# Kernel optimization log

Measured on AMD Instinct MI355X. Metric: run time of the kernel, lower is better.

The kernel has to match this reference:

```python
import jax, jax.numpy as jnp
import numpy as np

KH = KW = 3
PAD = 1

def _patches(x):
    # x: [B, C, H, W] -> periodic pad then 3x3 patches [B, C, KH, KW, H, W]
    B, C, H, W = x.shape
    xp = jnp.pad(x, ((0, 0), (0, 0), (PAD, PAD), (PAD, PAD)), mode='wrap')
    rows = []
    for i in range(KH):
        cols = [xp[:, :, i:i + H, j:j + W] for j in range(KW)]
        rows.append(jnp.stack(cols, axis=2))  # [B, C, KW, H, W]
    return jnp.stack(rows, axis=2)  # [B, C, KH, KW, H, W]

def setup_inputs() -> dict:
    key = jax.random.key(0)
    k1, k2, k3 = jax.random.split(key, 3)
    B, C, O, H, W = 16, 64, 64, 128, 128
    input = jax.random.normal(k1, (B, C, H, W), dtype=jnp.float32)
    weight = jax.random.normal(k2, (B, C * KH * KW, O), dtype=jnp.float32) * 0.05
    bias = jax.random.normal(k3, (B, O), dtype=jnp.float32) * 0.05
    return {"input": input, "weight": weight, "bias": bias}

def reference(input, weight, bias):
    B, C, H, W = input.shape
    O = weight.shape[-1]
    p = _patches(input)  # [B, C, KH, KW, H, W]
    w = weight.reshape(B, C, KH, KW, O)
    # per-sample dynamic conv: contract over (C, KH, KW)
    y = jnp.einsum('bcijhw,bcijo->bohw', p, w)
    return y + bias[:, :, None, None]
```

## Files before the change

kernel.cpp:

```cpp
#include <hip/hip_runtime.h>
#include <stdint.h>

#define B_N 16
#define C_N 64
#define O_N 64
#define H_N 128
#define W_N 128

typedef short bf16x8 __attribute__((ext_vector_type(8)));
typedef float f32x4 __attribute__((ext_vector_type(4)));
typedef unsigned short u16;
typedef u16 u16x4 __attribute__((ext_vector_type(4)));
typedef u16 u16x8 __attribute__((ext_vector_type(8)));

__device__ __forceinline__ u16 f2bf(float f) {
    uint32_t u = __float_as_uint(f);
    u += 0x7FFFu + ((u >> 16) & 1u);
    return (u16)(u >> 16);
}

__device__ __forceinline__ int swz(int w) { return (w & 7) << 4; }

__global__ __launch_bounds__(512, 2) void conv_main(const float* __restrict__ x,
                                                    const float* __restrict__ wt,
                                                    const float* __restrict__ bias,
                                                    float* __restrict__ y) {
    __shared__ u16 xl[6 * 128 * 64];

    const int lid = (blockIdx.x & 7) * 32 + (blockIdx.x >> 3);
    const int b   = lid >> 4;
    const int h0  = (lid & 15) * 8;
    const int tid = threadIdx.x;
    const int wid = tid >> 6;
    const int l   = tid & 63;
    const int wave_m = wid >> 1;
    const int wave_n = wid & 1;
    const int m0 = wave_m * 32;
    const int o0 = wave_n * 32;
    const int lr = l & 15;
    const int lg = l >> 4;

    const int w4 = tid & 31;
    const int cq = tid >> 5;
    const float* xb  = x  + (size_t)b * (64 * 128 * 128);
    const float* wtb = wt + (size_t)b * (576 * 64);

    auto ldrow = [&](int s, f32x4* d) {
        int hr = (h0 + s + 127) & 127;
        const float* src = xb + ((size_t)cq * 4 * 128 + hr) * 128 + w4 * 4;
        d[0] = *reinterpret_cast<const f32x4*>(src);
        d[1] = *reinterpret_cast<const f32x4*>(src + 16384);
        d[2] = *reinterpret_cast<const f32x4*>(src + 32768);
        d[3] = *reinterpret_cast<const f32x4*>(src + 49152);
    };
    auto wrrow = [&](int slot, const f32x4* d) {
#pragma unroll
        for (int j = 0; j < 4; ++j) {
            int w = w4 * 4 + j;
            u16x4 pk;
            pk.x = f2bf(d[0][j]); pk.y = f2bf(d[1][j]);
            pk.z = f2bf(d[2][j]); pk.w = f2bf(d[3][j]);
            int byte = slot * 16384 + w * 128 + ((cq * 8) ^ swz(w));
            *reinterpret_cast<u16x4*>(reinterpret_cast<char*>(xl) + byte) = pk;
        }
    };

    f32x4 s0[4], s1[4], s2[4], st[4];
    ldrow(0, s0); ldrow(1, s1); ldrow(2, s2);

    u16* wl = xl;
#pragma unroll
    for (int it = 0; it < 9; ++it) {
        int task = it * 512 + tid;
        int tl = task & 63;
        int of = (task >> 6) & 3;
        int cs = (task >> 8) & 1;
        int ij = task >> 9;
        const int o = of * 16 + (tl & 15);
        const int cbase = cs * 32 + (tl >> 4) * 8;
        u16x8 pk;
#pragma unroll
        for (int j8 = 0; j8 < 8; ++j8) {
            float v = wtb[(size_t)(cbase + j8) * 9 * 64 + (size_t)ij * 64 + o];
            pk[j8] = f2bf(v);
        }
        *reinterpret_cast<u16x8*>(wl + (size_t)task * 8) = pk;
    }
    __syncthreads();

    bf16x8 wreg[9][2][2];
#pragma unroll
    for (int ij = 0; ij < 9; ++ij)
#pragma unroll
        for (int cs = 0; cs < 2; ++cs)
#pragma unroll
            for (int nf = 0; nf < 2; ++nf)
                wreg[ij][cs][nf] = *reinterpret_cast<const bf16x8*>(
                    wl + (size_t)(((ij * 2 + cs) * 4 + wave_n * 2 + nf) * 64 + l) * 8);

    const float bv0 = bias[b * 64 + o0 + lr];
    const float bv1 = bias[b * 64 + o0 + 16 + lr];
    __syncthreads();

    wrrow(0, s0); wrrow(1, s1); wrrow(2, s2);
    ldrow(3, s0); ldrow(4, st);
    wrrow(3, s0);
    __syncthreads();

    int slA = 0;
#pragma unroll 1
    for (int r = 0; r < 8; ++r) {
        const int slB = (slA + 1 == 6) ? 0 : slA + 1;
        const int slC = (slB + 1 == 6) ? 0 : slB + 1;
        const int slW = (slC + 2 >= 6) ? slC + 2 - 6 : slC + 2;
        const int base0 = slA * 16384, base1 = slB * 16384, base2 = slC * 16384;

        f32x4 acc[2][2];
#pragma unroll
        for (int mf = 0; mf < 2; ++mf)
#pragma unroll
            for (int nf = 0; nf < 2; ++nf)
                acc[mf][nf] = (f32x4){0.f, 0.f, 0.f, 0.f};

#pragma unroll
        for (int ij = 0; ij < 9; ++ij) {
            if (ij == 0 && r < 6) wrrow(slW, st);
            if (ij == 3 && r < 5) ldrow(r + 5, st);

            const int i = ij / 3;
            const int jsh = ij % 3 - 1;
            const int rbase = (i == 0) ? base0 : (i == 1) ? base1 : base2;
#pragma unroll
            for (int cs = 0; cs < 2; ++cs) {
                const int cb = cs * 64 + lg * 16;
                bf16x8 afr[2];
#pragma unroll
                for (int mf = 0; mf < 2; ++mf) {
                    int w = (m0 + mf * 16 + lr + jsh + 128) & 127;
                    int byte = rbase + w * 128 + (cb ^ swz(w));
                    afr[mf] = *reinterpret_cast<const bf16x8*>(
                        reinterpret_cast<const char*>(xl) + byte);
                }
#pragma unroll
                for (int mf = 0; mf < 2; ++mf) {
                    acc[mf][0] = __builtin_amdgcn_mfma_f32_16x16x32_bf16(afr[mf], wreg[ij][cs][0], acc[mf][0], 0, 0, 0);
                    acc[mf][1] = __builtin_amdgcn_mfma_f32_16x16x32_bf16(afr[mf], wreg[ij][cs][1], acc[mf][1], 0, 0, 0);
                }
            }
        }

        const int h = h0 + r;
#pragma unroll
        for (int nf = 0; nf < 2; ++nf) {
            int o = o0 + nf * 16 + lr;
            float bv = nf ? bv1 : bv0;
#pragma unroll
            for (int mf = 0; mf < 2; ++mf) {
                int w0 = m0 + mf * 16 + lg * 4;
                float* dst = y + (((size_t)b * 64 + o) * 128 + h) * 128 + w0;
                f32x4 out;
                out[0] = acc[mf][nf][0] + bv;
                out[1] = acc[mf][nf][1] + bv;
                out[2] = acc[mf][nf][2] + bv;
                out[3] = acc[mf][nf][3] + bv;
                *reinterpret_cast<f32x4*>(dst) = out;
            }
        }

        if ((r & 1) && r < 7) __syncthreads();
        slA = slB;
    }
}

extern "C" void kernel_launch(void* const* d_in, const int* in_sizes, int n_in,
                              void* d_out, int out_size, void* d_ws, size_t ws_size,
                              hipStream_t stream) {
    const float* x    = (const float*)d_in[0];
    const float* wt   = (const float*)d_in[1];
    const float* bias = (const float*)d_in[2];
    float* y = (float*)d_out;
    (void)d_ws; (void)ws_size;

    hipLaunchKernelGGL(conv_main, dim3(B_N * H_N / 8), dim3(512), 0, stream,
                       x, wt, bias, y);
}
```

Before: 32.58 us.

## Reuse each staged input row across three output rows with rotating accumulators

Restructures the main loop to iterate over input rows instead of output rows. Each LDS-loaded A fragment feeds the MFMAs of up to three output rows, held in three rotating accumulator sets. This cuts LDS reads per output roughly threefold. It also fully unrolls the schedule and relaxes launch bounds to one block per SM, which raises register pressure and lowers occupancy.

```diff
diff --git a/kernel.cpp b/kernel.cpp
--- a/kernel.cpp
+++ b/kernel.cpp
@@ -21,7 +21,7 @@
 
 __device__ __forceinline__ int swz(int w) { return (w & 7) << 4; }
 
-__global__ __launch_bounds__(512, 2) void conv_main(const float* __restrict__ x,
+__global__ __launch_bounds__(512, 1) void conv_main(const float* __restrict__ x,
                                                     const float* __restrict__ wt,
                                                     const float* __restrict__ bias,
                                                     float* __restrict__ y) {
@@ -107,29 +107,25 @@
     wrrow(3, s0);
     __syncthreads();
 
-    int slA = 0;
-#pragma unroll 1
-    for (int r = 0; r < 8; ++r) {
-        const int slB = (slA + 1 == 6) ? 0 : slA + 1;
-        const int slC = (slB + 1 == 6) ? 0 : slB + 1;
-        const int slW = (slC + 2 >= 6) ? slC + 2 - 6 : slC + 2;
-        const int base0 = slA * 16384, base1 = slB * 16384, base2 = slC * 16384;
-
-        f32x4 acc[2][2];
+    f32x4 acc[3][2][2];
+#pragma unroll
+    for (int a = 0; a < 3; ++a)
 #pragma unroll
         for (int mf = 0; mf < 2; ++mf)
 #pragma unroll
             for (int nf = 0; nf < 2; ++nf)
-                acc[mf][nf] = (f32x4){0.f, 0.f, 0.f, 0.f};
-
-#pragma unroll
-        for (int ij = 0; ij < 9; ++ij) {
-            if (ij == 0 && r < 6) wrrow(slW, st);
-            if (ij == 3 && r < 5) ldrow(r + 5, st);
-
-            const int i = ij / 3;
-            const int jsh = ij % 3 - 1;
-            const int rbase = (i == 0) ? base0 : (i == 1) ? base1 : base2;
+                acc[a][mf][nf] = (f32x4){0.f, 0.f, 0.f, 0.f};
+
+#pragma unroll
+    for (int s = 0; s < 10; ++s) {
+        if (s <= 5) wrrow((s + 4) % 6, st);
+
+        const int rbase = (s % 6) * 16384;
+#pragma unroll
+        for (int jp = 0; jp < 3; ++jp) {
+            if (jp == 1 && s <= 4) ldrow(s + 5, st);
+
+            const int jsh = jp - 1;
 #pragma unroll
             for (int cs = 0; cs < 2; ++cs) {
                 const int cb = cs * 64 + lg * 16;
@@ -142,33 +138,53 @@
                         reinterpret_cast<const char*>(xl) + byte);
                 }
 #pragma unroll
-                for (int mf = 0; mf < 2; ++mf) {
-                    acc[mf][0] = __builtin_amdgcn_mfma_f32_16x16x32_bf16(afr[mf], wreg[ij][cs][0], acc[mf][0], 0, 0, 0);
-                    acc[mf][1] = __builtin_amdgcn_mfma_f32_16x16x32_bf16(afr[mf], wreg[ij][cs][1], acc[mf][1], 0, 0, 0);
+                for (int i = 0; i < 3; ++i) {
+                    const int r = s - i;
+                    if (r >= 0 && r <= 7) {
+                        const int a = r % 3;
+                        const int ij = i * 3 + jp;
+#pragma unroll
+                        for (int mf = 0; mf < 2; ++mf) {
+                            acc[a][mf][0] = __builtin_amdgcn_mfma_f32_16x16x32_bf16(
+                                afr[mf], wreg[ij][cs][0], acc[a][mf][0], 0, 0, 0);
+                            acc[a][mf][1] = __builtin_amdgcn_mfma_f32_16x16x32_bf16(
+                                afr[mf], wreg[ij][cs][1], acc[a][mf][1], 0, 0, 0);
+                        }
+                    }
                 }
             }
         }
 
-        const int h = h0 + r;
-#pragma unroll
-        for (int nf = 0; nf < 2; ++nf) {
-            int o = o0 + nf * 16 + lr;
-            float bv = nf ? bv1 : bv0;
-#pragma unroll
-            for (int mf = 0; mf < 2; ++mf) {
-                int w0 = m0 + mf * 16 + lg * 4;
-                float* dst = y + (((size_t)b * 64 + o) * 128 + h) * 128 + w0;
-                f32x4 out;
-                out[0] = acc[mf][nf][0] + bv;
-                out[1] = acc[mf][nf][1] + bv;
-                out[2] = acc[mf][nf][2] + bv;
-                out[3] = acc[mf][nf][3] + bv;
-                *reinterpret_cast<f32x4*>(dst) = out;
+        if (s >= 2) {
+            const int r = s - 2;
+            const int a = r % 3;
+            const int h = h0 + r;
+#pragma unroll
+            for (int nf = 0; nf < 2; ++nf) {
+                int o = o0 + nf * 16 + lr;
+                float bv = nf ? bv1 : bv0;
+#pragma unroll
+                for (int mf = 0; mf < 2; ++mf) {
+                    int w0 = m0 + mf * 16 + lg * 4;
+                    float* dst = y + (((size_t)b * 64 + o) * 128 + h) * 128 + w0;
+                    f32x4 out;
+                    out[0] = acc[a][mf][nf][0] + bv;
+                    out[1] = acc[a][mf][nf][1] + bv;
+                    out[2] = acc[a][mf][nf][2] + bv;
+                    out[3] = acc[a][mf][nf][3] + bv;
+                    *reinterpret_cast<f32x4*>(dst) = out;
+                }
             }
-        }
-
-        if ((r & 1) && r < 7) __syncthreads();
-        slA = slB;
+            if (r + 3 <= 7) {
+#pragma unroll
+                for (int mf = 0; mf < 2; ++mf)
+#pragma unroll
+                    for (int nf = 0; nf < 2; ++nf)
+                        acc[a][mf][nf] = (f32x4){0.f, 0.f, 0.f, 0.f};
+            }
+        }
+
+        if ((s & 1) && s < 9) __syncthreads();
     }
 }
 
```

Measured after the change: 55.82 us. 71.3% more time.

## Halve block to 4 waves, each computing all 64 output channels

Applied to the files above, without the earlier changes.

Block size drops from 512 to 256 threads. Each wave now covers 32 pixels by all 64 output channels instead of 32 by 32, which doubles weight registers and accumulators per wave. The row loads and stores are split into two halves per thread, and the weight staging loop runs 18 iterations. This raises per-thread register pressure (wreg grows to 72 bf16x8 vectors). Fewer waves are available to hide memory latency, in exchange for reusing each A fragment across more MFMAs.

```diff
diff --git a/kernel.cpp b/kernel.cpp
--- a/kernel.cpp
+++ b/kernel.cpp
@@ -21,7 +21,7 @@
 
 __device__ __forceinline__ int swz(int w) { return (w & 7) << 4; }
 
-__global__ __launch_bounds__(512, 2) void conv_main(const float* __restrict__ x,
+__global__ __launch_bounds__(256, 1) void conv_main(const float* __restrict__ x,
                                                     const float* __restrict__ wt,
                                                     const float* __restrict__ bias,
                                                     float* __restrict__ y) {
@@ -33,45 +33,49 @@
     const int tid = threadIdx.x;
     const int wid = tid >> 6;
     const int l   = tid & 63;
-    const int wave_m = wid >> 1;
-    const int wave_n = wid & 1;
-    const int m0 = wave_m * 32;
-    const int o0 = wave_n * 32;
-    const int lr = l & 15;
-    const int lg = l >> 4;
+    const int m0  = wid * 32;
+    const int lr  = l & 15;
+    const int lg  = l >> 4;
 
-    const int w4 = tid & 31;
-    const int cq = tid >> 5;
+    const int w4  = tid & 31;
+    const int cq2 = tid >> 5;
     const float* xb  = x  + (size_t)b * (64 * 128 * 128);
     const float* wtb = wt + (size_t)b * (576 * 64);
 
     auto ldrow = [&](int s, f32x4* d) {
         int hr = (h0 + s + 127) & 127;
-        const float* src = xb + ((size_t)cq * 4 * 128 + hr) * 128 + w4 * 4;
-        d[0] = *reinterpret_cast<const f32x4*>(src);
-        d[1] = *reinterpret_cast<const f32x4*>(src + 16384);
-        d[2] = *reinterpret_cast<const f32x4*>(src + 32768);
-        d[3] = *reinterpret_cast<const f32x4*>(src + 49152);
+#pragma unroll
+        for (int half = 0; half < 2; ++half) {
+            const float* src = xb + ((size_t)(cq2 * 2 + half) * 4 * 128 + hr) * 128 + w4 * 4;
+            d[half * 4 + 0] = *reinterpret_cast<const f32x4*>(src);
+            d[half * 4 + 1] = *reinterpret_cast<const f32x4*>(src + 16384);
+            d[half * 4 + 2] = *reinterpret_cast<const f32x4*>(src + 32768);
+            d[half * 4 + 3] = *reinterpret_cast<const f32x4*>(src + 49152);
+        }
     };
     auto wrrow = [&](int slot, const f32x4* d) {
 #pragma unroll
-        for (int j = 0; j < 4; ++j) {
-            int w = w4 * 4 + j;
-            u16x4 pk;
-            pk.x = f2bf(d[0][j]); pk.y = f2bf(d[1][j]);
-            pk.z = f2bf(d[2][j]); pk.w = f2bf(d[3][j]);
-            int byte = slot * 16384 + w * 128 + ((cq * 8) ^ swz(w));
-            *reinterpret_cast<u16x4*>(reinterpret_cast<char*>(xl) + byte) = pk;
+        for (int half = 0; half < 2; ++half) {
+            const int cq = cq2 * 2 + half;
+#pragma unroll
+            for (int j = 0; j < 4; ++j) {
+                int w = w4 * 4 + j;
+                u16x4 pk;
+                pk.x = f2bf(d[half * 4 + 0][j]); pk.y = f2bf(d[half * 4 + 1][j]);
+                pk.z = f2bf(d[half * 4 + 2][j]); pk.w = f2bf(d[half * 4 + 3][j]);
+                int byte = slot * 16384 + w * 128 + ((cq * 8) ^ swz(w));
+                *reinterpret_cast<u16x4*>(reinterpret_cast<char*>(xl) + byte) = pk;
+            }
         }
     };
 
-    f32x4 s0[4], s1[4], s2[4], st[4];
-    ldrow(0, s0); ldrow(1, s1); ldrow(2, s2);
+    f32x4 sA[8], sB[8], st[8];
+    ldrow(0, sA); ldrow(1, sB);
 
     u16* wl = xl;
 #pragma unroll
-    for (int it = 0; it < 9; ++it) {
-        int task = it * 512 + tid;
+    for (int it = 0; it < 18; ++it) {
+        int task = it * 256 + tid;
         int tl = task & 63;
         int of = (task >> 6) & 3;
         int cs = (task >> 8) & 1;
@@ -88,23 +92,24 @@
     }
     __syncthreads();
 
-    bf16x8 wreg[9][2][2];
+    bf16x8 wreg[9][2][4];
 #pragma unroll
     for (int ij = 0; ij < 9; ++ij)
 #pragma unroll
         for (int cs = 0; cs < 2; ++cs)
 #pragma unroll
-            for (int nf = 0; nf < 2; ++nf)
+            for (int nf = 0; nf < 4; ++nf)
                 wreg[ij][cs][nf] = *reinterpret_cast<const bf16x8*>(
-                    wl + (size_t)(((ij * 2 + cs) * 4 + wave_n * 2 + nf) * 64 + l) * 8);
+                    wl + (size_t)(((ij * 2 + cs) * 4 + nf) * 64 + l) * 8);
 
-    const float bv0 = bias[b * 64 + o0 + lr];
-    const float bv1 = bias[b * 64 + o0 + 16 + lr];
+    float bv[4];
+#pragma unroll
+    for (int nf = 0; nf < 4; ++nf) bv[nf] = bias[b * 64 + nf * 16 + lr];
     __syncthreads();
 
-    wrrow(0, s0); wrrow(1, s1); wrrow(2, s2);
-    ldrow(3, s0); ldrow(4, st);
-    wrrow(3, s0);
+    wrrow(0, sA); wrrow(1, sB);
+    ldrow(2, sA); ldrow(3, sB); ldrow(4, st);
+    wrrow(2, sA); wrrow(3, sB);
     __syncthreads();
 
     int slA = 0;
@@ -115,11 +120,11 @@
         const int slW = (slC + 2 >= 6) ? slC + 2 - 6 : slC + 2;
         const int base0 = slA * 16384, base1 = slB * 16384, base2 = slC * 16384;
 
-        f32x4 acc[2][2];
+        f32x4 acc[2][4];
 #pragma unroll
         for (int mf = 0; mf < 2; ++mf)
 #pragma unroll
-            for (int nf = 0; nf < 2; ++nf)
+            for (int nf = 0; nf < 4; ++nf)
                 acc[mf][nf] = (f32x4){0.f, 0.f, 0.f, 0.f};
 
 #pragma unroll
@@ -142,27 +147,27 @@
                         reinterpret_cast<const char*>(xl) + byte);
                 }
 #pragma unroll
-                for (int mf = 0; mf < 2; ++mf) {
-                    acc[mf][0] = __builtin_amdgcn_mfma_f32_16x16x32_bf16(afr[mf], wreg[ij][cs][0], acc[mf][0], 0, 0, 0);
-                    acc[mf][1] = __builtin_amdgcn_mfma_f32_16x16x32_bf16(afr[mf], wreg[ij][cs][1], acc[mf][1], 0, 0, 0);
-                }
+                for (int mf = 0; mf < 2; ++mf)
+#pragma unroll
+                    for (int nf = 0; nf < 4; ++nf)
+                        acc[mf][nf] = __builtin_amdgcn_mfma_f32_16x16x32_bf16(
+                            afr[mf], wreg[ij][cs][nf], acc[mf][nf], 0, 0, 0);
             }
         }
 
         const int h = h0 + r;
 #pragma unroll
-        for (int nf = 0; nf < 2; ++nf) {
-            int o = o0 + nf * 16 + lr;
-            float bv = nf ? bv1 : bv0;
+        for (int nf = 0; nf < 4; ++nf) {
+            int o = nf * 16 + lr;
 #pragma unroll
             for (int mf = 0; mf < 2; ++mf) {
                 int w0 = m0 + mf * 16 + lg * 4;
                 float* dst = y + (((size_t)b * 64 + o) * 128 + h) * 128 + w0;
                 f32x4 out;
-                out[0] = acc[mf][nf][0] + bv;
-                out[1] = acc[mf][nf][1] + bv;
-                out[2] = acc[mf][nf][2] + bv;
-                out[3] = acc[mf][nf][3] + bv;
+                out[0] = acc[mf][nf][0] + bv[nf];
+                out[1] = acc[mf][nf][1] + bv[nf];
+                out[2] = acc[mf][nf][2] + bv[nf];
+                out[3] = acc[mf][nf][3] + bv[nf];
                 *reinterpret_cast<f32x4*>(dst) = out;
             }
         }
@@ -181,6 +186,6 @@
     float* y = (float*)d_out;
     (void)d_ws; (void)ws_size;
 
-    hipLaunchKernelGGL(conv_main, dim3(B_N * H_N / 8), dim3(512), 0, stream,
+    hipLaunchKernelGGL(conv_main, dim3(B_N * H_N / 8), dim3(256), 0, stream,
                        x, wt, bias, y);
 }
```

Result: slower. 44.53 us (+36.7%).
